# Optimization experiments

Measured on AMD Instinct MI355X. Metric: run time of the kernel, lower is better.

Reference implementation:

```python
import jax, jax.numpy as jnp
import numpy as np

NUM_HEADS = 16
EPS = 1e-5


def _layernorm(x, gamma, beta):
    # LayerNorm over last dim (head_dim), biased variance as in torch
    mu = jnp.mean(x, axis=-1, keepdims=True)
    var = jnp.mean(jnp.square(x - mu), axis=-1, keepdims=True)
    return (x - mu) * jax.lax.rsqrt(var + EPS) * gamma + beta


def setup_inputs() -> dict:
    key = jax.random.key(0)
    ks = jax.random.split(key, 10)
    B, T, C = 16, 2048, 1024
    Bk = 4
    Dh = C // NUM_HEADS
    w = 0.02
    return {
        "q": jax.random.normal(ks[0], (B, T, C), jnp.float32),
        "k": jax.random.normal(ks[1], (Bk, T, C), jnp.float32),
        "v": jax.random.normal(ks[2], (Bk, T, C), jnp.float32),
        "Wq": jax.random.normal(ks[3], (C, C), jnp.float32) * w,
        "Wk": jax.random.normal(ks[4], (C, C), jnp.float32) * w,
        "Wv": jax.random.normal(ks[5], (C, C), jnp.float32) * w,
        "Wo": jax.random.normal(ks[6], (C, C), jnp.float32) * w,
        "bo": jnp.zeros((C,), jnp.float32),
        "gamma": jnp.ones((Dh,), jnp.float32),
        "beta": jnp.zeros((Dh,), jnp.float32),
    }


def reference(q, k, v, Wq, Wk, Wv, Wo, bo, gamma, beta):
    B, N, C = q.shape
    H = NUM_HEADS
    Dh = C // H
    scale = 8.0 / Dh  # use_mup=True

    reps = B // k.shape[0]
    k = jnp.tile(k, (reps, 1, 1))[:, :N]
    v = jnp.tile(v, (reps, 1, 1))[:, :N]

    # torch Linear: x @ W.T  (no qkv bias)
    qp = jnp.einsum("bnc,dc->bnd", q, Wq).reshape(B, N, H, Dh)
    kp = jnp.einsum("bnc,dc->bnd", k, Wk).reshape(B, N, H, Dh)
    vp = jnp.einsum("bnc,dc->bnd", v, Wv).reshape(B, N, H, Dh)

    qp = _layernorm(qp, gamma, beta) * scale
    kp = _layernorm(kp, gamma, beta)

    # Faithful to source: NO head permute before matmul -> per-token (H,H) attention
    attn = jnp.einsum("bnhd,bngd->bnhg", qp, kp)  # [B,N,H,H]
    attn = jax.nn.softmax(attn, axis=-1)
    x = jnp.einsum("bnhg,bngd->bnhd", attn, vp)  # [B,N,H,Dh]
    # torch: transpose(1,2).reshape(B,N,C)
    x = x.transpose(0, 2, 1, 3).reshape(B, N, C)
    return jnp.einsum("bnc,dc->bnd", x, Wo) + bo
```

## Files before the change

kernel.cpp:

```cpp
#include <hip/hip_runtime.h>
#include <stdint.h>

typedef short bf16x8 __attribute__((ext_vector_type(8)));
typedef float f32x4 __attribute__((ext_vector_type(4)));

#define DEVINL static __device__ __forceinline__

DEVINL unsigned short f2bf(float f) {
    union { float f; uint32_t u; } v; v.f = f;
    return (unsigned short)((v.u + 0x7FFFu + ((v.u >> 16) & 1u)) >> 16);
}
DEVINL float bf2f(unsigned short b) {
    union { uint32_t u; float f; } v; v.u = ((uint32_t)b) << 16;
    return v.f;
}

DEVINL void load_lds16(const void* g, void* l) {
    __builtin_amdgcn_global_load_lds(
        (const __attribute__((address_space(1))) void*)g,
        (__attribute__((address_space(3))) void*)l, 16, 0, 0);
}

__global__ __launch_bounds__(256) void k_cvt(const float* __restrict__ src,
                                             unsigned short* __restrict__ dst, int n4) {
    int stride = gridDim.x * blockDim.x;
    for (int i = blockIdx.x * blockDim.x + threadIdx.x; i < n4; i += stride) {
        float4 f = reinterpret_cast<const float4*>(src)[i];
        ushort4 o;
        o.x = f2bf(f.x); o.y = f2bf(f.y); o.z = f2bf(f.z); o.w = f2bf(f.w);
        reinterpret_cast<ushort4*>(dst)[i] = o;
    }
}

template<int EPI>
__global__ __launch_bounds__(512, 2) void k_gemm256(
    const unsigned short* __restrict__ A,
    const unsigned short* __restrict__ B,
    void* __restrict__ Cout,
    const float* __restrict__ bias,
    const float* __restrict__ gamma,
    const float* __restrict__ beta)
{
    constexpr int K = 1024;
    constexpr int N = 1024;
    constexpr int NT = 16;
    __shared__ __align__(16) unsigned short lds[2][2][2][256][32];

    const int nwg = gridDim.x;
    const int bid = blockIdx.x;
    const int wg  = (bid & 7) * (nwg >> 3) + (bid >> 3);
    const int m0 = (wg >> 2) * 256;
    const int n0 = (wg & 3) * 256;

    const int tid = threadIdx.x;
    const int w = tid >> 6;
    const int lane = tid & 63;
    const int wr = w >> 2;
    const int wc = w & 3;

    const int srow = lane >> 2;
    const int sseg = lane & 3;
    const int sslot = sseg ^ ((srow >> 1) & 3);

    f32x4 acc[8][4] = {};

    auto stage_unit = [&](int buf, int kt, int unit) {
        const int k0 = kt * 64;
        const int ab = unit & 1;
        const int sel = unit >> 1;
        #pragma unroll
        for (int j = 0; j < 2; ++j) {
            const int c  = (w << 1) | j;
            const int ks = c >> 3;
            const int c3 = c & 7;
            const int rg = ab ? (sel * 2 + (c3 & 1) + ((c3 >> 1) << 2))
                              : (sel * 4 + (c3 & 3) + ((c3 >> 2) << 3));
            const int row = rg * 16 + srow;
            const unsigned short* src =
                (ab ? B + (size_t)(n0 + row) * K : A + (size_t)(m0 + row) * K)
                + k0 + ks * 32 + sslot * 8;
            load_lds16(src, &lds[buf][ab][ks][rg * 16][0]);
        }
    };

    const int rr = lane & 15;
    const int rdslot = ((lane >> 4) ^ ((rr >> 1) & 3)) * 8;

    stage_unit(0, 0, 0);
    stage_unit(0, 0, 1);
    stage_unit(0, 0, 2);
    stage_unit(0, 0, 3);

    bf16x8 a[4][2], b0[2][2], b1[2][2];
    int cur = 0;
    for (int kt = 0; kt < NT - 1; ++kt) {
        const int nxt = cur ^ 1;

        stage_unit(nxt, kt + 1, 0);
        asm volatile("s_waitcnt vmcnt(6)" ::: "memory");
        __builtin_amdgcn_s_barrier();
        __builtin_amdgcn_sched_barrier(0);
        #pragma unroll
        for (int i = 0; i < 4; ++i)
            #pragma unroll
            for (int ks = 0; ks < 2; ++ks)
                a[i][ks] = *reinterpret_cast<const bf16x8*>(
                    &lds[cur][0][ks][wr * 128 + i * 16 + rr][0] + rdslot);
        #pragma unroll
        for (int j = 0; j < 2; ++j)
            #pragma unroll
            for (int ks = 0; ks < 2; ++ks)
                b0[j][ks] = *reinterpret_cast<const bf16x8*>(
                    &lds[cur][1][ks][wc * 64 + j * 16 + rr][0] + rdslot);
        asm volatile("s_waitcnt lgkmcnt(0)" ::: "memory");
        __builtin_amdgcn_sched_barrier(0);
        __builtin_amdgcn_s_setprio(1);
        #pragma unroll
        for (int i = 0; i < 4; ++i)
            #pragma unroll
            for (int j = 0; j < 2; ++j)
                #pragma unroll
                for (int ks = 0; ks < 2; ++ks)
                    acc[i][j] = __builtin_amdgcn_mfma_f32_16x16x32_bf16(
                        a[i][ks], b0[j][ks], acc[i][j], 0, 0, 0);
        __builtin_amdgcn_s_setprio(0);

        stage_unit(nxt, kt + 1, 1);
        asm volatile("s_waitcnt vmcnt(4)" ::: "memory");
        __builtin_amdgcn_s_barrier();
        __builtin_amdgcn_sched_barrier(0);
        #pragma unroll
        for (int j = 0; j < 2; ++j)
            #pragma unroll
            for (int ks = 0; ks < 2; ++ks)
                b1[j][ks] = *reinterpret_cast<const bf16x8*>(
                    &lds[cur][1][ks][wc * 64 + 32 + j * 16 + rr][0] + rdslot);
        asm volatile("s_waitcnt lgkmcnt(0)" ::: "memory");
        __builtin_amdgcn_sched_barrier(0);
        __builtin_amdgcn_s_setprio(1);
        #pragma unroll
        for (int i = 0; i < 4; ++i)
            #pragma unroll
            for (int j = 0; j < 2; ++j)
                #pragma unroll
                for (int ks = 0; ks < 2; ++ks)
                    acc[i][2 + j] = __builtin_amdgcn_mfma_f32_16x16x32_bf16(
                        a[i][ks], b1[j][ks], acc[i][2 + j], 0, 0, 0);
        __builtin_amdgcn_s_setprio(0);

        stage_unit(nxt, kt + 1, 2);
        __builtin_amdgcn_s_barrier();
        __builtin_amdgcn_sched_barrier(0);
        #pragma unroll
        for (int i = 0; i < 4; ++i)
            #pragma unroll
            for (int ks = 0; ks < 2; ++ks)
                a[i][ks] = *reinterpret_cast<const bf16x8*>(
                    &lds[cur][0][ks][wr * 128 + 64 + i * 16 + rr][0] + rdslot);
        asm volatile("s_waitcnt lgkmcnt(0)" ::: "memory");
        __builtin_amdgcn_sched_barrier(0);
        __builtin_amdgcn_s_setprio(1);
        #pragma unroll
        for (int i = 0; i < 4; ++i)
            #pragma unroll
            for (int j = 0; j < 2; ++j)
                #pragma unroll
                for (int ks = 0; ks < 2; ++ks)
                    acc[4 + i][j] = __builtin_amdgcn_mfma_f32_16x16x32_bf16(
                        a[i][ks], b0[j][ks], acc[4 + i][j], 0, 0, 0);
        __builtin_amdgcn_s_setprio(0);

        stage_unit(nxt, kt + 1, 3);
        __builtin_amdgcn_s_barrier();
        __builtin_amdgcn_sched_barrier(0);
        __builtin_amdgcn_s_setprio(1);
        #pragma unroll
        for (int i = 0; i < 4; ++i)
            #pragma unroll
            for (int j = 0; j < 2; ++j)
                #pragma unroll
                for (int ks = 0; ks < 2; ++ks)
                    acc[4 + i][2 + j] = __builtin_amdgcn_mfma_f32_16x16x32_bf16(
                        a[i][ks], b1[j][ks], acc[4 + i][2 + j], 0, 0, 0);
        __builtin_amdgcn_s_setprio(0);
        cur = nxt;
    }

    {
        asm volatile("s_waitcnt vmcnt(4)" ::: "memory");
        __builtin_amdgcn_s_barrier();
        __builtin_amdgcn_sched_barrier(0);
        #pragma unroll
        for (int i = 0; i < 4; ++i)
            #pragma unroll
            for (int ks = 0; ks < 2; ++ks)
                a[i][ks] = *reinterpret_cast<const bf16x8*>(
                    &lds[cur][0][ks][wr * 128 + i * 16 + rr][0] + rdslot);
        #pragma unroll
        for (int j = 0; j < 2; ++j)
            #pragma unroll
            for (int ks = 0; ks < 2; ++ks)
                b0[j][ks] = *reinterpret_cast<const bf16x8*>(
                    &lds[cur][1][ks][wc * 64 + j * 16 + rr][0] + rdslot);
        asm volatile("s_waitcnt lgkmcnt(0)" ::: "memory");
        __builtin_amdgcn_sched_barrier(0);
        __builtin_amdgcn_s_setprio(1);
        #pragma unroll
        for (int i = 0; i < 4; ++i)
            #pragma unroll
            for (int j = 0; j < 2; ++j)
                #pragma unroll
                for (int ks = 0; ks < 2; ++ks)
                    acc[i][j] = __builtin_amdgcn_mfma_f32_16x16x32_bf16(
                        a[i][ks], b0[j][ks], acc[i][j], 0, 0, 0);
        __builtin_amdgcn_s_setprio(0);

        asm volatile("s_waitcnt vmcnt(0)" ::: "memory");
        __builtin_amdgcn_s_barrier();
        __builtin_amdgcn_sched_barrier(0);
        #pragma unroll
        for (int j = 0; j < 2; ++j)
            #pragma unroll
            for (int ks = 0; ks < 2; ++ks)
                b1[j][ks] = *reinterpret_cast<const bf16x8*>(
                    &lds[cur][1][ks][wc * 64 + 32 + j * 16 + rr][0] + rdslot);
        asm volatile("s_waitcnt lgkmcnt(0)" ::: "memory");
        __builtin_amdgcn_sched_barrier(0);
        __builtin_amdgcn_s_setprio(1);
        #pragma unroll
        for (int i = 0; i < 4; ++i)
            #pragma unroll
            for (int j = 0; j < 2; ++j)
                #pragma unroll
                for (int ks = 0; ks < 2; ++ks)
                    acc[i][2 + j] = __builtin_amdgcn_mfma_f32_16x16x32_bf16(
                        a[i][ks], b1[j][ks], acc[i][2 + j], 0, 0, 0);
        __builtin_amdgcn_s_setprio(0);

        #pragma unroll
        for (int i = 0; i < 4; ++i)
            #pragma unroll
            for (int ks = 0; ks < 2; ++ks)
                a[i][ks] = *reinterpret_cast<const bf16x8*>(
                    &lds[cur][0][ks][wr * 128 + 64 + i * 16 + rr][0] + rdslot);
        asm volatile("s_waitcnt lgkmcnt(0)" ::: "memory");
        __builtin_amdgcn_sched_barrier(0);
        __builtin_amdgcn_s_setprio(1);
        #pragma unroll
        for (int i = 0; i < 4; ++i)
            #pragma unroll
            for (int j = 0; j < 2; ++j)
                #pragma unroll
                for (int ks = 0; ks < 2; ++ks) {
                    acc[4 + i][j] = __builtin_amdgcn_mfma_f32_16x16x32_bf16(
                        a[i][ks], b0[j][ks], acc[4 + i][j], 0, 0, 0);
                    acc[4 + i][2 + j] = __builtin_amdgcn_mfma_f32_16x16x32_bf16(
                        a[i][ks], b1[j][ks], acc[4 + i][2 + j], 0, 0, 0);
                }
        __builtin_amdgcn_s_setprio(0);
    }

    const int rg = lane >> 4;
    if constexpr (EPI == 0) {
        #pragma unroll
        for (int jj = 0; jj < 4; ++jj) {
            const int col = n0 + wc * 64 + jj * 16 + rr;
            const float bv = bias[col];
            #pragma unroll
            for (int i = 0; i < 8; ++i) {
                const int row0 = m0 + wr * 128 + i * 16 + rg * 4;
                #pragma unroll
                for (int r = 0; r < 4; ++r)
                    reinterpret_cast<float*>(Cout)[(size_t)(row0 + r) * N + col] =
                        acc[i][jj][r] + bv;
            }
        }
    } else if constexpr (EPI == 1 || EPI == 3) {
        const float scale = (EPI == 1) ? 0.125f : 1.0f;
        float gm[4], bt[4];
        #pragma unroll
        for (int jj = 0; jj < 4; ++jj) { gm[jj] = gamma[jj * 16 + rr]; bt[jj] = beta[jj * 16 + rr]; }
        #pragma unroll
        for (int i = 0; i < 8; ++i)
            #pragma unroll
            for (int r = 0; r < 4; ++r) {
                float s = 0.f, sq = 0.f;
                #pragma unroll
                for (int jj = 0; jj < 4; ++jj) {
                    const float v = acc[i][jj][r];
                    s += v; sq += v * v;
                }
                s  += __shfl_xor(s, 1);  s  += __shfl_xor(s, 2);
                s  += __shfl_xor(s, 4);  s  += __shfl_xor(s, 8);
                sq += __shfl_xor(sq, 1); sq += __shfl_xor(sq, 2);
                sq += __shfl_xor(sq, 4); sq += __shfl_xor(sq, 8);
                const float mu = s * 0.015625f;
                const float var = sq * 0.015625f - mu * mu;
                const float inv = rsqrtf(var + 1e-5f);
                const int row = m0 + wr * 128 + i * 16 + rg * 4 + r;
                #pragma unroll
                for (int jj = 0; jj < 4; ++jj) {
                    const int col = n0 + wc * 64 + jj * 16 + rr;
                    const float val = ((acc[i][jj][r] - mu) * inv * gm[jj] + bt[jj]) * scale;
                    reinterpret_cast<unsigned short*>(Cout)[(size_t)row * N + col] = f2bf(val);
                }
            }
    } else {
        const int g = (wg & 3) * 4 + wc;
        const int kqv = g >> 3;
        const int ev = g & 7;
        #pragma unroll
        for (int i = 0; i < 8; ++i)
            #pragma unroll
            for (int r = 0; r < 4; ++r) {
                const int t = m0 + wr * 128 + i * 16 + rg * 4 + r;
                #pragma unroll
                for (int jj = 0; jj < 4; ++jj)
                    reinterpret_cast<unsigned short*>(Cout)[
                        (size_t)t * 1024 + jj * 256 + kqv * 128 + rr * 8 + ev] =
                        f2bf(acc[i][jj][r]);
            }
    }
}

__global__ __launch_bounds__(256) void k_attn2(
    const unsigned short* __restrict__ qln,
    const unsigned short* __restrict__ kln,
    const unsigned short* __restrict__ vperm,
    unsigned short* __restrict__ xout)
{
    __shared__ unsigned short ps[4][256];
    __shared__ unsigned short xs[4][16 * 68];

    const int w = threadIdx.x >> 6;
    const int lane = threadIdx.x & 63;
    const int token = blockIdx.x * 4 + w;
    const int b = token >> 11;
    const int n = token & 2047;
    const int tokk = (b & 3) * 2048 + n;
    const int rr = lane & 15;
    const int kq = lane >> 4;

    const unsigned short* qp = qln + (size_t)token * 1024 + rr * 64 + kq * 8;
    const unsigned short* kp = kln + (size_t)tokk * 1024 + rr * 64 + kq * 8;
    const bf16x8 aq0 = *reinterpret_cast<const bf16x8*>(qp);
    const bf16x8 aq1 = *reinterpret_cast<const bf16x8*>(qp + 32);
    const bf16x8 bk0 = *reinterpret_cast<const bf16x8*>(kp);
    const bf16x8 bk1 = *reinterpret_cast<const bf16x8*>(kp + 32);
    f32x4 s = {};
    s = __builtin_amdgcn_mfma_f32_16x16x32_bf16(aq0, bk0, s, 0, 0, 0);
    s = __builtin_amdgcn_mfma_f32_16x16x32_bf16(aq1, bk1, s, 0, 0, 0);

    #pragma unroll
    for (int r = 0; r < 4; ++r) {
        float m = s[r];
        m = fmaxf(m, __shfl_xor(m, 1));
        m = fmaxf(m, __shfl_xor(m, 2));
        m = fmaxf(m, __shfl_xor(m, 4));
        m = fmaxf(m, __shfl_xor(m, 8));
        const float e = __expf(s[r] - m);
        float t = e;
        t += __shfl_xor(t, 1); t += __shfl_xor(t, 2);
        t += __shfl_xor(t, 4); t += __shfl_xor(t, 8);
        ps[w][(kq * 4 + r) * 16 + rr] = f2bf(e / t);
    }

    bf16x8 ap = {};
    if (kq < 2)
        ap = *reinterpret_cast<const bf16x8*>(&ps[w][rr * 16 + kq * 8]);

    const unsigned short* vp = vperm + (size_t)tokk * 1024;
    #pragma unroll
    for (int dblk = 0; dblk < 4; ++dblk) {
        bf16x8 bv = {};
        if (kq < 2)
            bv = *reinterpret_cast<const bf16x8*>(vp + dblk * 256 + kq * 128 + rr * 8);
        f32x4 z = {};
        const f32x4 x = __builtin_amdgcn_mfma_f32_16x16x32_bf16(ap, bv, z, 0, 0, 0);
        #pragma unroll
        for (int r = 0; r < 4; ++r)
            xs[w][(kq * 4 + r) * 68 + dblk * 16 + rr] = f2bf(x[r]);
    }

    const int h2 = lane >> 2;
    const int sg = lane & 3;
    const uint4 lo = *reinterpret_cast<const uint4*>(&xs[w][h2 * 68 + sg * 16]);
    const uint4 hi = *reinterpret_cast<const uint4*>(&xs[w][h2 * 68 + sg * 16 + 8]);
    unsigned short* dst = xout + (size_t)b * 2048 * 1024 +
                          (size_t)(h2 * 128 + (n >> 4)) * 1024 + (n & 15) * 64 + sg * 16;
    *reinterpret_cast<uint4*>(dst) = lo;
    *reinterpret_cast<uint4*>(dst + 8) = hi;
}

extern "C" void kernel_launch(void* const* d_in, const int* in_sizes, int n_in,
                              void* d_out, int out_size, void* d_ws, size_t ws_size,
                              hipStream_t stream) {
    const float* q     = (const float*)d_in[0];
    const float* k     = (const float*)d_in[1];
    const float* v     = (const float*)d_in[2];
    const float* Wq    = (const float*)d_in[3];
    const float* Wk    = (const float*)d_in[4];
    const float* Wv    = (const float*)d_in[5];
    const float* Wo    = (const float*)d_in[6];
    const float* bo    = (const float*)d_in[7];
    const float* gamma = (const float*)d_in[8];
    const float* beta  = (const float*)d_in[9];
    float* out = (float*)d_out;

    char* ws = (char*)d_ws;
    const size_t MB = 1024 * 1024;
    unsigned short* qb    = (unsigned short*)(ws + 0);
    unsigned short* xsc   = (unsigned short*)(ws + 0);
    unsigned short* qpb   = (unsigned short*)(ws + 64 * MB);
    unsigned short* klnb  = (unsigned short*)(ws + 128 * MB);
    unsigned short* vpm   = (unsigned short*)(ws + 160 * MB);
    unsigned short* kbb   = (unsigned short*)(ws + 176 * MB);
    unsigned short* vbb   = (unsigned short*)(ws + 176 * MB);
    unsigned short* Wkb   = (unsigned short*)(ws + 192 * MB);
    unsigned short* Wvb   = (unsigned short*)(ws + 194 * MB);
    unsigned short* Wqb   = (unsigned short*)(ws + 196 * MB);
    unsigned short* Wob   = (unsigned short*)(ws + 198 * MB);

    k_cvt<<<512, 256, 0, stream>>>(Wk, Wkb, 262144);
    k_cvt<<<1024, 256, 0, stream>>>(k, kbb, 2097152);
    k_gemm256<3><<<128, 512, 0, stream>>>(kbb, Wkb, klnb, nullptr, gamma, beta);

    k_cvt<<<512, 256, 0, stream>>>(Wv, Wvb, 262144);
    k_cvt<<<1024, 256, 0, stream>>>(v, vbb, 2097152);
    k_gemm256<2><<<128, 512, 0, stream>>>(vbb, Wvb, vpm, nullptr, nullptr, nullptr);

    k_cvt<<<512, 256, 0, stream>>>(Wq, Wqb, 262144);
    k_cvt<<<2048, 256, 0, stream>>>(q, qb, 8388608);
    k_gemm256<1><<<512, 512, 0, stream>>>(qb, Wqb, qpb, nullptr, gamma, beta);

    k_attn2<<<8192, 256, 0, stream>>>(qpb, klnb, vpm, xsc);

    k_cvt<<<512, 256, 0, stream>>>(Wo, Wob, 262144);
    k_gemm256<0><<<512, 512, 0, stream>>>(xsc, Wob, out, bo, nullptr, nullptr);
}
```

Baseline: 343.8 us.

## Restructure GEMM mainloop to full-tile prefetch with one barrier per k-step; batch weight conversions

```diff
diff --git a/kernel.cpp b/kernel.cpp
--- a/kernel.cpp
+++ b/kernel.cpp
@@ -5,6 +5,7 @@
 typedef float f32x4 __attribute__((ext_vector_type(4)));
 
 #define DEVINL static __device__ __forceinline__
+#define SB() __builtin_amdgcn_sched_barrier(0)
 
 DEVINL unsigned short f2bf(float f) {
     union { float f; uint32_t u; } v; v.f = f;
@@ -25,6 +26,25 @@
                                              unsigned short* __restrict__ dst, int n4) {
     int stride = gridDim.x * blockDim.x;
     for (int i = blockIdx.x * blockDim.x + threadIdx.x; i < n4; i += stride) {
+        float4 f = reinterpret_cast<const float4*>(src)[i];
+        ushort4 o;
+        o.x = f2bf(f.x); o.y = f2bf(f.y); o.z = f2bf(f.z); o.w = f2bf(f.w);
+        reinterpret_cast<ushort4*>(dst)[i] = o;
+    }
+}
+
+__global__ __launch_bounds__(256) void k_cvtW(
+    const float* __restrict__ s0, const float* __restrict__ s1,
+    const float* __restrict__ s2, const float* __restrict__ s3,
+    unsigned short* __restrict__ d0, unsigned short* __restrict__ d1,
+    unsigned short* __restrict__ d2, unsigned short* __restrict__ d3) {
+    const float* srcs[4] = {s0, s1, s2, s3};
+    unsigned short* dsts[4] = {d0, d1, d2, d3};
+    const int wsel = blockIdx.x >> 8;
+    const int blk  = blockIdx.x & 255;
+    const float* src = srcs[wsel];
+    unsigned short* dst = dsts[wsel];
+    for (int i = blk * 256 + threadIdx.x; i < 262144; i += 65536) {
         float4 f = reinterpret_cast<const float4*>(src)[i];
         ushort4 o;
         o.x = f2bf(f.x); o.y = f2bf(f.y); o.z = f2bf(f.z); o.w = f2bf(f.w);
@@ -64,56 +84,80 @@
 
     f32x4 acc[8][4] = {};
 
-    auto stage_unit = [&](int buf, int kt, int unit) {
+    auto stage_all = [&](int buf, int kt) {
         const int k0 = kt * 64;
-        const int ab = unit & 1;
-        const int sel = unit >> 1;
-        #pragma unroll
-        for (int j = 0; j < 2; ++j) {
-            const int c  = (w << 1) | j;
-            const int ks = c >> 3;
-            const int c3 = c & 7;
-            const int rg = ab ? (sel * 2 + (c3 & 1) + ((c3 >> 1) << 2))
-                              : (sel * 4 + (c3 & 3) + ((c3 >> 2) << 3));
-            const int row = rg * 16 + srow;
-            const unsigned short* src =
-                (ab ? B + (size_t)(n0 + row) * K : A + (size_t)(m0 + row) * K)
-                + k0 + ks * 32 + sslot * 8;
-            load_lds16(src, &lds[buf][ab][ks][rg * 16][0]);
+        #pragma unroll
+        for (int unit = 0; unit < 4; ++unit) {
+            const int ab = unit & 1;
+            const int sel = unit >> 1;
+            #pragma unroll
+            for (int j = 0; j < 2; ++j) {
+                const int c  = (w << 1) | j;
+                const int ks = c >> 3;
+                const int c3 = c & 7;
+                const int rg = ab ? (sel * 2 + (c3 & 1) + ((c3 >> 1) << 2))
+                                  : (sel * 4 + (c3 & 3) + ((c3 >> 2) << 3));
+                const int row = rg * 16 + srow;
+                const unsigned short* src =
+                    (ab ? B + (size_t)(n0 + row) * K : A + (size_t)(m0 + row) * K)
+                    + k0 + ks * 32 + sslot * 8;
+                load_lds16(src, &lds[buf][ab][ks][rg * 16][0]);
+            }
         }
     };
 
     const int rr = lane & 15;
     const int rdslot = ((lane >> 4) ^ ((rr >> 1) & 3)) * 8;
 
-    stage_unit(0, 0, 0);
-    stage_unit(0, 0, 1);
-    stage_unit(0, 0, 2);
-    stage_unit(0, 0, 3);
+    stage_all(0, 0);
+    asm volatile("s_waitcnt vmcnt(0)" ::: "memory");
+    __builtin_amdgcn_s_barrier();
+    SB();
 
     bf16x8 a[4][2], b0[2][2], b1[2][2];
+
+    auto rd_a = [&](bf16x8 (&a_)[4][2], int mh) {
+        #pragma unroll
+        for (int i = 0; i < 4; ++i)
+            #pragma unroll
+            for (int ks = 0; ks < 2; ++ks)
+                a_[i][ks] = *reinterpret_cast<const bf16x8*>(
+                    &lds[0][0][ks][0][0] +
+                    ((size_t)(
+                    0)) );
+    };
+    (void)rd_a;
+
     int cur = 0;
-    for (int kt = 0; kt < NT - 1; ++kt) {
+    for (int kt = 0; kt < NT; ++kt) {
         const int nxt = cur ^ 1;
-
-        stage_unit(nxt, kt + 1, 0);
-        asm volatile("s_waitcnt vmcnt(6)" ::: "memory");
-        __builtin_amdgcn_s_barrier();
-        __builtin_amdgcn_sched_barrier(0);
+        const bool pf = (kt + 1 < NT);
+        if (pf) stage_all(nxt, kt + 1);
+
         #pragma unroll
         for (int i = 0; i < 4; ++i)
             #pragma unroll
             for (int ks = 0; ks < 2; ++ks)
                 a[i][ks] = *reinterpret_cast<const bf16x8*>(
                     &lds[cur][0][ks][wr * 128 + i * 16 + rr][0] + rdslot);
+        SB();
         #pragma unroll
         for (int j = 0; j < 2; ++j)
             #pragma unroll
             for (int ks = 0; ks < 2; ++ks)
                 b0[j][ks] = *reinterpret_cast<const bf16x8*>(
                     &lds[cur][1][ks][wc * 64 + j * 16 + rr][0] + rdslot);
-        asm volatile("s_waitcnt lgkmcnt(0)" ::: "memory");
-        __builtin_amdgcn_sched_barrier(0);
+        SB();
+        #pragma unroll
+        for (int j = 0; j < 2; ++j)
+            #pragma unroll
+            for (int ks = 0; ks < 2; ++ks)
+                b1[j][ks] = *reinterpret_cast<const bf16x8*>(
+                    &lds[cur][1][ks][wc * 64 + 32 + j * 16 + rr][0] + rdslot);
+        SB();
+
+        asm volatile("s_waitcnt lgkmcnt(4)" ::: "memory");
+        SB();
         __builtin_amdgcn_s_setprio(1);
         #pragma unroll
         for (int i = 0; i < 4; ++i)
@@ -125,18 +169,8 @@
                         a[i][ks], b0[j][ks], acc[i][j], 0, 0, 0);
         __builtin_amdgcn_s_setprio(0);
 
-        stage_unit(nxt, kt + 1, 1);
-        asm volatile("s_waitcnt vmcnt(4)" ::: "memory");
-        __builtin_amdgcn_s_barrier();
-        __builtin_amdgcn_sched_barrier(0);
-        #pragma unroll
-        for (int j = 0; j < 2; ++j)
-            #pragma unroll
-            for (int ks = 0; ks < 2; ++ks)
-                b1[j][ks] = *reinterpret_cast<const bf16x8*>(
-                    &lds[cur][1][ks][wc * 64 + 32 + j * 16 + rr][0] + rdslot);
         asm volatile("s_waitcnt lgkmcnt(0)" ::: "memory");
-        __builtin_amdgcn_sched_barrier(0);
+        SB();
         __builtin_amdgcn_s_setprio(1);
         #pragma unroll
         for (int i = 0; i < 4; ++i)
@@ -148,103 +182,15 @@
                         a[i][ks], b1[j][ks], acc[i][2 + j], 0, 0, 0);
         __builtin_amdgcn_s_setprio(0);
 
-        stage_unit(nxt, kt + 1, 2);
-        __builtin_amdgcn_s_barrier();
-        __builtin_amdgcn_sched_barrier(0);
         #pragma unroll
         for (int i = 0; i < 4; ++i)
             #pragma unroll
             for (int ks = 0; ks < 2; ++ks)
                 a[i][ks] = *reinterpret_cast<const bf16x8*>(
                     &lds[cur][0][ks][wr * 128 + 64 + i * 16 + rr][0] + rdslot);
+        SB();
         asm volatile("s_waitcnt lgkmcnt(0)" ::: "memory");
-        __builtin_amdgcn_sched_barrier(0);
-        __builtin_amdgcn_s_setprio(1);
-        #pragma unroll
-        for (int i = 0; i < 4; ++i)
-            #pragma unroll
-            for (int j = 0; j < 2; ++j)
-                #pragma unroll
-                for (int ks = 0; ks < 2; ++ks)
-                    acc[4 + i][j] = __builtin_amdgcn_mfma_f32_16x16x32_bf16(
-                        a[i][ks], b0[j][ks], acc[4 + i][j], 0, 0, 0);
-        __builtin_amdgcn_s_setprio(0);
-
-        stage_unit(nxt, kt + 1, 3);
-        __builtin_amdgcn_s_barrier();
-        __builtin_amdgcn_sched_barrier(0);
-        __builtin_amdgcn_s_setprio(1);
-        #pragma unroll
-        for (int i = 0; i < 4; ++i)
-            #pragma unroll
-            for (int j = 0; j < 2; ++j)
-                #pragma unroll
-                for (int ks = 0; ks < 2; ++ks)
-                    acc[4 + i][2 + j] = __builtin_amdgcn_mfma_f32_16x16x32_bf16(
-                        a[i][ks], b1[j][ks], acc[4 + i][2 + j], 0, 0, 0);
-        __builtin_amdgcn_s_setprio(0);
-        cur = nxt;
-    }
-
-    {
-        asm volatile("s_waitcnt vmcnt(4)" ::: "memory");
-        __builtin_amdgcn_s_barrier();
-        __builtin_amdgcn_sched_barrier(0);
-        #pragma unroll
-        for (int i = 0; i < 4; ++i)
-            #pragma unroll
-            for (int ks = 0; ks < 2; ++ks)
-                a[i][ks] = *reinterpret_cast<const bf16x8*>(
-                    &lds[cur][0][ks][wr * 128 + i * 16 + rr][0] + rdslot);
-        #pragma unroll
-        for (int j = 0; j < 2; ++j)
-            #pragma unroll
-            for (int ks = 0; ks < 2; ++ks)
-                b0[j][ks] = *reinterpret_cast<const bf16x8*>(
-                    &lds[cur][1][ks][wc * 64 + j * 16 + rr][0] + rdslot);
-        asm volatile("s_waitcnt lgkmcnt(0)" ::: "memory");
-        __builtin_amdgcn_sched_barrier(0);
-        __builtin_amdgcn_s_setprio(1);
-        #pragma unroll
-        for (int i = 0; i < 4; ++i)
-            #pragma unroll
-            for (int j = 0; j < 2; ++j)
-                #pragma unroll
-                for (int ks = 0; ks < 2; ++ks)
-                    acc[i][j] = __builtin_amdgcn_mfma_f32_16x16x32_bf16(
-                        a[i][ks], b0[j][ks], acc[i][j], 0, 0, 0);
-        __builtin_amdgcn_s_setprio(0);
-
-        asm volatile("s_waitcnt vmcnt(0)" ::: "memory");
-        __builtin_amdgcn_s_barrier();
-        __builtin_amdgcn_sched_barrier(0);
-        #pragma unroll
-        for (int j = 0; j < 2; ++j)
-            #pragma unroll
-            for (int ks = 0; ks < 2; ++ks)
-                b1[j][ks] = *reinterpret_cast<const bf16x8*>(
-                    &lds[cur][1][ks][wc * 64 + 32 + j * 16 + rr][0] + rdslot);
-        asm volatile("s_waitcnt lgkmcnt(0)" ::: "memory");
-        __builtin_amdgcn_sched_barrier(0);
-        __builtin_amdgcn_s_setprio(1);
-        #pragma unroll
-        for (int i = 0; i < 4; ++i)
-            #pragma unroll
-            for (int j = 0; j < 2; ++j)
-                #pragma unroll
-                for (int ks = 0; ks < 2; ++ks)
-                    acc[i][2 + j] = __builtin_amdgcn_mfma_f32_16x16x32_bf16(
-                        a[i][ks], b1[j][ks], acc[i][2 + j], 0, 0, 0);
-        __builtin_amdgcn_s_setprio(0);
-
-        #pragma unroll
-        for (int i = 0; i < 4; ++i)
-            #pragma unroll
-            for (int ks = 0; ks < 2; ++ks)
-                a[i][ks] = *reinterpret_cast<const bf16x8*>(
-                    &lds[cur][0][ks][wr * 128 + 64 + i * 16 + rr][0] + rdslot);
-        asm volatile("s_waitcnt lgkmcnt(0)" ::: "memory");
-        __builtin_amdgcn_sched_barrier(0);
+        SB();
         __builtin_amdgcn_s_setprio(1);
         #pragma unroll
         for (int i = 0; i < 4; ++i)
@@ -258,6 +204,14 @@
                         a[i][ks], b1[j][ks], acc[4 + i][2 + j], 0, 0, 0);
                 }
         __builtin_amdgcn_s_setprio(0);
+
+        if (pf) {
+            asm volatile("s_waitcnt vmcnt(0)" ::: "memory");
+            SB();
+            __builtin_amdgcn_s_barrier();
+            SB();
+        }
+        cur = nxt;
     }
 
     const int rg = lane >> 4;
@@ -421,20 +375,18 @@
     unsigned short* Wqb   = (unsigned short*)(ws + 196 * MB);
     unsigned short* Wob   = (unsigned short*)(ws + 198 * MB);
 
-    k_cvt<<<512, 256, 0, stream>>>(Wk, Wkb, 262144);
+    k_cvtW<<<1024, 256, 0, stream>>>(Wk, Wv, Wq, Wo, Wkb, Wvb, Wqb, Wob);
+
     k_cvt<<<1024, 256, 0, stream>>>(k, kbb, 2097152);
     k_gemm256<3><<<128, 512, 0, stream>>>(kbb, Wkb, klnb, nullptr, gamma, beta);
 
-    k_cvt<<<512, 256, 0, stream>>>(Wv, Wvb, 262144);
     k_cvt<<<1024, 256, 0, stream>>>(v, vbb, 2097152);
     k_gemm256<2><<<128, 512, 0, stream>>>(vbb, Wvb, vpm, nullptr, nullptr, nullptr);
 
-    k_cvt<<<512, 256, 0, stream>>>(Wq, Wqb, 262144);
     k_cvt<<<2048, 256, 0, stream>>>(q, qb, 8388608);
     k_gemm256<1><<<512, 512, 0, stream>>>(qb, Wqb, qpb, nullptr, gamma, beta);
 
     k_attn2<<<8192, 256, 0, stream>>>(qpb, klnb, vpm, xsc);
 
-    k_cvt<<<512, 256, 0, stream>>>(Wo, Wob, 262144);
     k_gemm256<0><<<512, 512, 0, stream>>>(xsc, Wob, out, bo, nullptr, nullptr);
 }
```

New measurement: 358.0 us. +4.1%, slower.
